# Performance work log

Measured on AMD Instinct MI355X. Metric: run time of the kernel, lower is better.

## Reference

```python
import jax, jax.numpy as jnp
import numpy as np

D_MODEL = 2048
H = 16
D_K = D_MODEL // H


def setup_inputs() -> dict:
    key = jax.random.key(0)
    ks = jax.random.split(key, 9)
    b, n, d = 2, 2048, D_MODEL
    s = 1.0 / np.sqrt(d)
    return {
        "x": jax.random.normal(ks[0], (b, n, d), jnp.float32),
        "Wq": jax.random.normal(ks[1], (d, d), jnp.float32) * s,
        "bq": jax.random.normal(ks[2], (d,), jnp.float32) * 0.01,
        "Wk": jax.random.normal(ks[3], (d, d), jnp.float32) * s,
        "bk": jax.random.normal(ks[4], (d,), jnp.float32) * 0.01,
        "Wv": jax.random.normal(ks[5], (d, d), jnp.float32) * s,
        "bv": jax.random.normal(ks[6], (d,), jnp.float32) * 0.01,
        "Wo": jax.random.normal(ks[7], (d, d), jnp.float32) * s,
        "bo": jax.random.normal(ks[8], (d,), jnp.float32) * 0.01,
    }


def reference(x, Wq, bq, Wk, bk, Wv, bv, Wo, bo):
    b, n, d = x.shape
    h, dk = H, D_K

    def split_heads(t):
        return t.reshape(b, n, h, dk).transpose(0, 2, 1, 3)  # (b,h,n,dk)

    q = split_heads(x @ Wq + bq)
    k = split_heads(x @ Wk + bk)
    v = split_heads(x @ Wv + bv)

    scores = jnp.einsum("bhqd,bhkd->bhqk", q, k) / jnp.sqrt(jnp.float32(dk))
    causal = jnp.tril(jnp.ones((n, n), dtype=bool))  # (n,n)
    scores = jnp.where(causal[None, None], scores, -jnp.inf)
    attn = jax.nn.softmax(scores, axis=-1)  # dropout = identity (eval)

    out = jnp.einsum("bhqk,bhkd->bhqd", attn, v)
    out = out.transpose(0, 2, 1, 3).reshape(b, n, d)
    return out @ Wo + bo
```

## Files before the change

### kernel.cpp

```cpp
#include <hip/hip_runtime.h>

typedef unsigned short u16;
typedef unsigned int u32;
typedef __attribute__((ext_vector_type(8))) short short8;
typedef __attribute__((ext_vector_type(4))) float f32x4;
typedef __attribute__((ext_vector_type(16))) float f32x16;
typedef __attribute__((ext_vector_type(4))) u16 u16x4;
typedef __attribute__((ext_vector_type(4))) u32 u32x4;

#define QK_SCALE 0.12751736915185197f

__device__ __forceinline__ u16 f2bf(float f) {
  u32 u = __builtin_bit_cast(u32, f);
  u = u + 0x7FFFu + ((u >> 16) & 1u);
  return (u16)(u >> 16);
}

__device__ __forceinline__ void async_copy16(const void* g, void* l) {
  __builtin_amdgcn_global_load_lds(
      (const __attribute__((address_space(1))) u32*)g,
      (__attribute__((address_space(3))) u32*)l, 16, 0, 0);
}

#define VMCNT(n) asm volatile("s_waitcnt vmcnt(" #n ")" ::: "memory")

__global__ __launch_bounds__(256) void cast_x_kernel(const float* __restrict__ x,
                                                     u16* __restrict__ xb, int n) {
  int i = (blockIdx.x * 256 + threadIdx.x) * 8;
  if (i >= n) return;
  float4 a = *(const float4*)(x + i);
  float4 b = *(const float4*)(x + i + 4);
  short8 o;
  o[0] = (short)f2bf(a.x); o[1] = (short)f2bf(a.y);
  o[2] = (short)f2bf(a.z); o[3] = (short)f2bf(a.w);
  o[4] = (short)f2bf(b.x); o[5] = (short)f2bf(b.y);
  o[6] = (short)f2bf(b.z); o[7] = (short)f2bf(b.w);
  *(short8*)(xb + i) = o;
}

__global__ __launch_bounds__(256) void transW_kernel(
    const float* __restrict__ W0, const float* __restrict__ W1,
    const float* __restrict__ W2, const float* __restrict__ W3,
    u16* __restrict__ O0, u16* __restrict__ O1, u16* __restrict__ O2, u16* __restrict__ O3) {
  const float* Ws[4] = {W0, W1, W2, W3};
  u16* Os[4] = {O0, O1, O2, O3};
  const float* W = Ws[blockIdx.z];
  u16* O = Os[blockIdx.z];

  __shared__ float T[64][65];
  int t = threadIdx.x;
  int k0 = blockIdx.y * 64, n0 = blockIdx.x * 64;
  int r = t >> 4, c = (t & 15) * 4;
#pragma unroll
  for (int i = 0; i < 4; ++i) {
    float4 v = *(const float4*)&W[(size_t)(k0 + r + i * 16) * 2048 + n0 + c];
    T[r + i * 16][c + 0] = v.x; T[r + i * 16][c + 1] = v.y;
    T[r + i * 16][c + 2] = v.z; T[r + i * 16][c + 3] = v.w;
  }
  __syncthreads();
#pragma unroll
  for (int i = 0; i < 4; ++i) {
    int nn = r + i * 16;
    u16x4 o;
    o[0] = f2bf(T[c + 0][nn]); o[1] = f2bf(T[c + 1][nn]);
    o[2] = f2bf(T[c + 2][nn]); o[3] = f2bf(T[c + 3][nn]);
    *(u16x4*)&O[(size_t)(n0 + nn) * 2048 + k0 + c] = o;
  }
}

__global__ __launch_bounds__(512, 1) void gemm256_kernel(
    const u16* __restrict__ A, const u16* __restrict__ W,
    const float* __restrict__ b0, const float* __restrict__ b1, const float* __restrict__ b2,
    u16* __restrict__ oq, u16* __restrict__ ok, u16* __restrict__ ovt) {
  __shared__ __align__(16) u16 SM[67584];

  int t = threadIdx.x;
  int lane = t & 63, w = t >> 6;
  int wm = w >> 2, wn = w & 3;
  int g = lane >> 4, lr = lane & 15;
  int m0 = blockIdx.y * 256, n0 = blockIdx.x * 256;

  const u16* AsrcB = A + (size_t)(m0 + (t >> 3)) * 2048 + ((t & 7) ^ ((t >> 3) & 7)) * 8;
  const u16* BsrcB = W + (size_t)(n0 + (t >> 3)) * 2048 + ((t & 7) ^ ((t >> 3) & 7)) * 8;
  int t8 = t * 8;

  int ko0 = (g ^ (lr & 7)) * 8;
  int ko1 = ((4 + g) ^ (lr & 7)) * 8;
  int aoff[8], boff[4];
#pragma unroll
  for (int mf = 0; mf < 8; ++mf) aoff[mf] = (wm * 128 + mf * 16 + lr) * 64;
#pragma unroll
  for (int nf = 0; nf < 4; ++nf) boff[nf] = (wn * 64 + nf * 16 + lr) * 64;

  f32x4 acc[8][4] = {};
  short8 af[2][2], bfr[4][2];

#define SA(b, j, tl) \
  async_copy16(AsrcB + (size_t)(j) * 131072 + (tl) * 64, (void*)(SM + (b) * 32768 + (j) * 4096 + t8))
#define SB(b, j, tl) \
  async_copy16(BsrcB + (size_t)(j) * 131072 + (tl) * 64, \
               (void*)(SM + (b) * 32768 + 16384 + (j) * 4096 + t8))

#define PHASE(hbuf, q, STAGE_OPS, VM_OP)                                        \
  {                                                                             \
    const u16* Ab = SM + (hbuf) * 32768;                                        \
    const u16* Bb = Ab + 16384;                                                 \
    af[0][0] = *(const short8*)&Ab[aoff[2 * (q)] + ko0];                        \
    af[0][1] = *(const short8*)&Ab[aoff[2 * (q)] + ko1];                        \
    af[1][0] = *(const short8*)&Ab[aoff[2 * (q) + 1] + ko0];                    \
    af[1][1] = *(const short8*)&Ab[aoff[2 * (q) + 1] + ko1];                    \
    if ((q) == 0) {                                                             \
      _Pragma("unroll") for (int nf = 0; nf < 4; ++nf) {                        \
        bfr[nf][0] = *(const short8*)&Bb[boff[nf] + ko0];                       \
        bfr[nf][1] = *(const short8*)&Bb[boff[nf] + ko1];                       \
      }                                                                         \
    }                                                                           \
    STAGE_OPS;                                                                  \
    __builtin_amdgcn_s_barrier();                                               \
    asm volatile("s_waitcnt lgkmcnt(0)" ::: "memory");                          \
    __builtin_amdgcn_sched_barrier(0);                                          \
    __builtin_amdgcn_s_setprio(1);                                              \
    _Pragma("unroll") for (int kk = 0; kk < 2; ++kk)                            \
        _Pragma("unroll") for (int m2 = 0; m2 < 2; ++m2)                        \
            _Pragma("unroll") for (int nf = 0; nf < 4; ++nf)                    \
                acc[2 * (q) + m2][nf] = __builtin_amdgcn_mfma_f32_16x16x32_bf16(\
                    af[m2][kk], bfr[nf][kk], acc[2 * (q) + m2][nf], 0, 0, 0);   \
    __builtin_amdgcn_s_setprio(0);                                              \
    VM_OP;                                                                      \
    __builtin_amdgcn_s_barrier();                                               \
  }

  SB(0, 0, 0); SB(0, 1, 0); SB(0, 2, 0); SB(0, 3, 0);
  SA(0, 0, 0); SA(0, 2, 0); SA(0, 1, 0); SA(0, 3, 0);
  SB(1, 0, 1); SB(1, 1, 1); SB(1, 2, 1); SB(1, 3, 1);
  SA(1, 0, 1); SA(1, 2, 1);
  VMCNT(6);
  __builtin_amdgcn_s_barrier();

  for (int i = 0; i < 16; ++i) {
    bool more = i < 15;
    int t1 = 2 * i + 1, t2 = 2 * i + 2, t3 = 2 * i + 3;
    PHASE(0, 0, { SA(1, 1, t1); SA(1, 3, t1); }, {});
    PHASE(0, 1, { if (more) { SB(0, 0, t2); SB(0, 1, t2); } }, {});
    PHASE(0, 2, { if (more) { SB(0, 2, t2); SB(0, 3, t2); } }, {});
    PHASE(0, 3, { if (more) { SA(0, 0, t2); SA(0, 2, t2); } },
          { if (more) { VMCNT(6); } else { VMCNT(0); } });
    PHASE(1, 0, { if (more) { SA(0, 1, t2); SA(0, 3, t2); } }, {});
    PHASE(1, 1, { if (more) { SB(1, 0, t3); SB(1, 1, t3); } }, {});
    PHASE(1, 2, { if (more) { SB(1, 2, t3); SB(1, 3, t3); } }, {});
    PHASE(1, 3, { if (more) { SA(1, 0, t3); SA(1, 2, t3); } },
          { if (more) { VMCNT(6); } else { VMCNT(0); } });
  }
#undef PHASE
#undef SA
#undef SB

  int zsel = n0 >> 11;
  const float* bias = (zsel == 0) ? b0 : (zsel == 1) ? b1 : b2;
  bool isV = (zsel == 2);

#pragma unroll
  for (int mf = 0; mf < 8; ++mf) {
#pragma unroll
    for (int nf = 0; nf < 4; ++nf) {
      int colc = wn * 64 + nf * 16 + lr;
      float bv = bias[(n0 + colc) & 2047];
#pragma unroll
      for (int i = 0; i < 4; ++i) {
        int token = wm * 128 + mf * 16 + 4 * g + i;
        u16 v = f2bf(acc[mf][nf][i] + bv);
        if (isV) SM[colc * 264 + token] = v;
        else SM[token * 264 + colc] = v;
      }
    }
  }
  __syncthreads();

  if (!isV) {
    u16* outb = (zsel == 0) ? oq : ok;
#pragma unroll
    for (int it = 0; it < 16; ++it) {
      int id = t + 512 * it;
      int token = id >> 5, c8 = (id & 31) * 8;
      short8 v = *(const short8*)&SM[token * 264 + c8];
      int rr = m0 + token;
      int colg = ((n0 + c8) & 2047);
      int b = rr >> 11, np = rr & 2047, h = colg >> 7, dk = colg & 127;
      *(short8*)&outb[((size_t)(b * 16 + h) * 2048 + np) * 128 + dk] = v;
    }
  } else {
#pragma unroll
    for (int it = 0; it < 16; ++it) {
      int id = t + 512 * it;
      int colc = id >> 5, t8k = (id & 31) * 8;
      short8 v = *(const short8*)&SM[colc * 264 + t8k];
      int rr = m0 + t8k;
      int vcol = (n0 - 4096) + colc;
      int b = rr >> 11, np = rr & 2047, h = vcol >> 7, dk = vcol & 127;
      *(short8*)&ovt[(((size_t)(b * 16 + h) * 128 + dk) * 2048) + np] = v;
    }
  }
}

__global__ __launch_bounds__(512, 2) void gemmO_kernel(
    const u16* __restrict__ A, const u16* __restrict__ W,
    const float* __restrict__ bias, float* __restrict__ of) {
  __shared__ __align__(16) u16 SM[73728];

  int t = threadIdx.x;
  int lane = t & 63, w = t >> 6;
  int wm = w >> 2, wn = w & 3;
  int g = lane >> 4, lr = lane & 15;
  int m0 = blockIdx.y * 128, n0 = blockIdx.x * 256;

  int sArow = ((t >> 8) << 6) + ((t >> 3) & 31);
  int c8A = (t & 7) ^ ((t >> 3) & 7);
  const u16* Asrc = A + (size_t)(m0 + sArow) * 2048 + c8A * 8;
  int rB = t >> 3;
  int c8B = (t & 7) ^ (rB & 7);
  const u16* Bsrc = W + (size_t)(n0 + rB) * 2048 + c8B * 8;

  int ko0 = (g ^ (lr & 7)) * 8;
  int ko1 = ((4 + g) ^ (lr & 7)) * 8;
  int offA[4], offB[4];
#pragma unroll
  for (int mf = 0; mf < 4; ++mf)
    offA[mf] = (mf >> 1) * 4096 + wm * 2048 + ((mf & 1) * 16 + lr) * 64;
#pragma unroll
  for (int nf = 0; nf < 4; ++nf)
    offB[nf] = 8192 + (wn >> 1) * 8192 + ((wn & 1) * 64 + nf * 16 + lr) * 64;

  f32x4 acc[4][4] = {};

#define STG_A(sbuf, mh, kt) \
  async_copy16(Asrc + (mh) * 65536 + (kt), (void*)(SM + (sbuf) + (mh) * 4096 + t * 8))
#define STG_B(sbuf, half, kt)                                                 \
  do {                                                                        \
    async_copy16(Bsrc + (half) * 262144 + (kt),                               \
                 (void*)(SM + (sbuf) + 8192 + (half) * 8192 + t * 8));        \
    async_copy16(Bsrc + (half) * 262144 + 131072 + (kt),                      \
                 (void*)(SM + (sbuf) + 8192 + (half) * 8192 + 4096 + t * 8)); \
  } while (0)

  STG_A(0, 0, 0); STG_B(0, 0, 0);
  STG_A(0, 1, 0); STG_B(0, 1, 0);
  STG_A(24576, 0, 64); STG_B(24576, 0, 64);
  STG_A(24576, 1, 64); STG_B(24576, 1, 64);
  VMCNT(6);
  __builtin_amdgcn_s_barrier();

  u32 cb = 0, sb = 49152;
  for (int tt = 0; tt < 32; ++tt) {
    int kt2 = (tt + 2) << 6;
    bool stg = tt < 30;
    const u16* Bu = SM + cb;

    short8 af[2][2], bfr[4][2];
#pragma unroll
    for (int m2 = 0; m2 < 2; ++m2) {
      af[m2][0] = *(const short8*)&Bu[offA[m2] + ko0];
      af[m2][1] = *(const short8*)&Bu[offA[m2] + ko1];
    }
#pragma unroll
    for (int nf = 0; nf < 4; ++nf) {
      bfr[nf][0] = *(const short8*)&Bu[offB[nf] + ko0];
      bfr[nf][1] = *(const short8*)&Bu[offB[nf] + ko1];
    }
    if (stg) { STG_A(sb, 0, kt2); STG_B(sb, 0, kt2); }
    __builtin_amdgcn_s_barrier();
    asm volatile("s_waitcnt lgkmcnt(0)" ::: "memory");
    __builtin_amdgcn_sched_barrier(0);
    __builtin_amdgcn_s_setprio(1);
#pragma unroll
    for (int kk = 0; kk < 2; ++kk)
#pragma unroll
      for (int m2 = 0; m2 < 2; ++m2)
#pragma unroll
        for (int nf = 0; nf < 4; ++nf)
          acc[m2][nf] =
              __builtin_amdgcn_mfma_f32_16x16x32_bf16(af[m2][kk], bfr[nf][kk], acc[m2][nf], 0, 0, 0);
    __builtin_amdgcn_s_setprio(0);
    __builtin_amdgcn_s_barrier();

#pragma unroll
    for (int m2 = 0; m2 < 2; ++m2) {
      af[m2][0] = *(const short8*)&Bu[offA[2 + m2] + ko0];
      af[m2][1] = *(const short8*)&Bu[offA[2 + m2] + ko1];
    }
    if (stg) { STG_A(sb, 1, kt2); STG_B(sb, 1, kt2); }
    __builtin_amdgcn_s_barrier();
    asm volatile("s_waitcnt lgkmcnt(0)" ::: "memory");
    __builtin_amdgcn_sched_barrier(0);
    __builtin_amdgcn_s_setprio(1);
#pragma unroll
    for (int kk = 0; kk < 2; ++kk)
#pragma unroll
      for (int m2 = 0; m2 < 2; ++m2)
#pragma unroll
        for (int nf = 0; nf < 4; ++nf)
          acc[2 + m2][nf] = __builtin_amdgcn_mfma_f32_16x16x32_bf16(af[m2][kk], bfr[nf][kk],
                                                                    acc[2 + m2][nf], 0, 0, 0);
    __builtin_amdgcn_s_setprio(0);
    if (tt < 30) { VMCNT(6); } else { VMCNT(0); }
    __builtin_amdgcn_s_barrier();

    cb += 24576; if (cb == 73728) cb = 0;
    sb += 24576; if (sb == 73728) sb = 0;
  }
#undef STG_A
#undef STG_B

#pragma unroll
  for (int mf = 0; mf < 4; ++mf) {
#pragma unroll
    for (int nf = 0; nf < 4; ++nf) {
      int col = n0 + wn * 64 + nf * 16 + lr;
      float bv = bias[col];
#pragma unroll
      for (int i = 0; i < 4; ++i) {
        int rr = m0 + wm * 64 + mf * 16 + 4 * g + i;
        of[(size_t)rr * 2048 + col] = acc[mf][nf][i] + bv;
      }
    }
  }
}

__global__ __launch_bounds__(256, 2) void attn_kernel(
    const u16* __restrict__ Q, const u16* __restrict__ K, const u16* __restrict__ Vt,
    u16* __restrict__ ctx) {
  int bh = blockIdx.y;
  int q0 = (int)(gridDim.x - 1 - blockIdx.x) * 128;
  int t = threadIdx.x, lane = t & 63, w = t >> 6;
  int h = lane >> 5;
  int ql = lane & 31;
  int q0w = q0 + w * 32;
  int qg = q0w + ql;

  const u16* Qb = Q + (size_t)bh * 262144;
  const u16* Kb = K + (size_t)bh * 262144;
  const u16* Vb = Vt + (size_t)bh * 262144;

  __shared__ __align__(16) u16 SM[32768];

  short8 qf[8];
  {
    const u16* qrow = Qb + (size_t)qg * 128 + 8 * h;
#pragma unroll
    for (int kk = 0; kk < 8; ++kk) qf[kk] = *(const short8*)(qrow + 16 * kk);
  }

  f32x16 acc[4] = {};
  float m = -1e30f, lsum = 0.f;

  int nt = (q0 + 128) >> 6;
  int wave_max = q0w + 31;

  auto STAGE = [&](int buf, int kv0) {
    u16* Ksb = SM + buf * 16384;
    u16* Vsb = Ksb + 8192;
#pragma unroll
    for (int it = 0; it < 4; ++it) {
      int p = t + 256 * it;
      int row = p >> 4;
      int c = (p & 15) ^ (row & 15);
      async_copy16(Kb + (size_t)(kv0 + row) * 128 + c * 8, (void*)(Ksb + p * 8));
      async_copy16(Vb + (size_t)(2 * row + (c >> 3)) * 2048 + kv0 + (c & 7) * 8,
                   (void*)(Vsb + p * 8));
    }
  };

  STAGE(0, 0);
  __syncthreads();

  for (int step = 0; step < nt; ++step) {
    int kv0 = step << 6;
    int cur = step & 1;
    if (step + 1 < nt) STAGE(cur ^ 1, (step + 1) << 6);

    if (kv0 <= wave_max) {
      const u16* Ksb = SM + cur * 16384;
      const u16* Vsb = Ksb + 8192;

      f32x16 s0 = {}, s1 = {};
      __builtin_amdgcn_s_setprio(1);
#pragma unroll
      for (int kk = 0; kk < 8; ++kk) {
        int c = (2 * kk + h) ^ (ql & 15);
        short8 kf0 = *(const short8*)&Ksb[ql * 128 + c * 8];
        s0 = __builtin_amdgcn_mfma_f32_32x32x16_bf16(kf0, qf[kk], s0, 0, 0, 0);
        short8 kf1 = *(const short8*)&Ksb[(32 + ql) * 128 + c * 8];
        s1 = __builtin_amdgcn_mfma_f32_32x32x16_bf16(kf1, qf[kk], s1, 0, 0, 0);
      }
      __builtin_amdgcn_s_setprio(0);

      if (kv0 + 63 > q0w) {
#pragma unroll
        for (int r = 0; r < 16; ++r) {
          int slot = (r & 3) + 8 * (r >> 2) + 4 * h;
          if (kv0 + slot > qg) s0[r] = -1e30f;
          if (kv0 + 32 + slot > qg) s1[r] = -1e30f;
        }
      }

      float tm = fmaxf(s0[0], s1[0]);
#pragma unroll
      for (int r = 1; r < 16; ++r) tm = fmaxf(tm, fmaxf(s0[r], s1[r]));
      tm = fmaxf(tm, __shfl_xor(tm, 32));
      tm *= QK_SCALE;

      if (__any(tm > m + 8.0f)) {
        float mn = fmaxf(m, tm);
        float rr = exp2f(m - mn);
        m = mn;
        lsum *= rr;
#pragma unroll
        for (int d = 0; d < 4; ++d)
#pragma unroll
          for (int i = 0; i < 16; ++i) acc[d][i] *= rr;
      }

      float rs = 0.f;
#pragma unroll
      for (int r = 0; r < 16; ++r) {
        s0[r] = exp2f(fmaf(s0[r], QK_SCALE, -m));
        s1[r] = exp2f(fmaf(s1[r], QK_SCALE, -m));
        rs += s0[r] + s1[r];
      }
      rs += __shfl_xor(rs, 32);
      lsum += rs;

      u32 up0[8], up1[8];
#pragma unroll
      for (int mi = 0; mi < 8; ++mi) {
        asm("v_cvt_pk_bf16_f32 %0, %1, %2" : "=v"(up0[mi]) : "v"(s0[2 * mi]), "v"(s0[2 * mi + 1]));
        asm("v_cvt_pk_bf16_f32 %0, %1, %2" : "=v"(up1[mi]) : "v"(s1[2 * mi]), "v"(s1[2 * mi + 1]));
      }

#pragma unroll
      for (int g16 = 0; g16 < 4; ++g16) {
        int Qd = g16 & 1;
        u32 c0 = (g16 < 2) ? up0[4 * Qd + 0] : up1[4 * Qd + 0];
        u32 c1 = (g16 < 2) ? up0[4 * Qd + 1] : up1[4 * Qd + 1];
        u32 c2 = (g16 < 2) ? up0[4 * Qd + 2] : up1[4 * Qd + 2];
        u32 c3 = (g16 < 2) ? up0[4 * Qd + 3] : up1[4 * Qd + 3];
        u32 d0 = __shfl_xor(c0, 32), d1 = __shfl_xor(c1, 32);
        u32 d2 = __shfl_xor(c2, 32), d3 = __shfl_xor(c3, 32);
        u32x4 paw;
        paw[0] = h ? d2 : c0;
        paw[1] = h ? d3 : c1;
        paw[2] = h ? c2 : d0;
        paw[3] = h ? c3 : d1;
        short8 pa = __builtin_bit_cast(short8, paw);
        __builtin_amdgcn_s_setprio(1);
#pragma unroll
        for (int d = 0; d < 4; ++d) {
          int dk = 32 * d + ql;
          int prow = dk >> 1;
          int lch = (dk & 1) * 8 + 2 * g16 + h;
          int slot = lch ^ (prow & 15);
          short8 vf = *(const short8*)&Vsb[prow * 128 + slot * 8];
          acc[d] = __builtin_amdgcn_mfma_f32_32x32x16_bf16(vf, pa, acc[d], 0, 0, 0);
        }
        __builtin_amdgcn_s_setprio(0);
      }
    }
    __syncthreads();
  }

  u16* Ot = SM + w * 4352;
  float inv = 1.f / lsum;
#pragma unroll
  for (int d = 0; d < 4; ++d)
#pragma unroll
    for (int r = 0; r < 16; ++r) {
      int dk = 32 * d + (r & 3) + 8 * (r >> 2) + 4 * h;
      Ot[ql * 136 + dk] = f2bf(acc[d][r] * inv);
    }
  __syncthreads();
  int b = bh >> 4, hh = bh & 15;
#pragma unroll
  for (int it = 0; it < 8; ++it) {
    int p = lane + 64 * it;
    int row = p >> 4, ch = p & 15;
    short8 v = *(const short8*)&Ot[row * 136 + ch * 8];
    *(short8*)(ctx + ((size_t)(b * 2048 + q0 + w * 32 + row)) * 2048 + hh * 128 + ch * 8) = v;
  }
}

extern "C" void kernel_launch(void* const* d_in, const int* in_sizes, int n_in,
                              void* d_out, int out_size, void* d_ws, size_t ws_size,
                              hipStream_t stream) {
  const float* x = (const float*)d_in[0];
  const float* Wq = (const float*)d_in[1];
  const float* bq = (const float*)d_in[2];
  const float* Wk = (const float*)d_in[3];
  const float* bk = (const float*)d_in[4];
  const float* Wv = (const float*)d_in[5];
  const float* bv = (const float*)d_in[6];
  const float* Wo = (const float*)d_in[7];
  const float* bo = (const float*)d_in[8];
  float* out = (float*)d_out;

  u16* xb = (u16*)d_ws;
  u16* WTq = xb + 8388608;
  u16* WTk = WTq + 4194304;
  u16* WTv = WTk + 4194304;
  u16* WTo = WTv + 4194304;
  u16* Qs = WTo + 4194304;
  u16* Ks = Qs + 8388608;
  u16* Vt = Ks + 8388608;
  u16* ctx = Vt + 8388608;

  cast_x_kernel<<<4096, 256, 0, stream>>>(x, xb, 8388608);
  transW_kernel<<<dim3(32, 32, 4), 256, 0, stream>>>(Wq, Wk, Wv, Wo, WTq, WTk, WTv, WTo);
  gemm256_kernel<<<dim3(24, 16), 512, 0, stream>>>(xb, WTq, bq, bk, bv, Qs, Ks, Vt);
  attn_kernel<<<dim3(16, 32), 256, 0, stream>>>(Qs, Ks, Vt, ctx);
  gemmO_kernel<<<dim3(8, 32), 512, 0, stream>>>(ctx, WTo, bo, out);
}
```

Baseline: 266.4 us.

## Shrink QKV GEMM tile to 256x192 to balance grid across CUs

The fused QKV projection GEMM now uses 256x192 tiles instead of 256x256, launching 512 blocks instead of 384 with a smaller LDS footprint and launch bounds that allow two blocks per CU. The aim is to fill the 256 CUs in whole waves and improve occupancy. Because tiles can now straddle the Q/K/V boundaries, the epilogue writes Q and K directly from registers with scalar stores and stages only the V columns through LDS for the transpose. The cost is lower arithmetic intensity per tile and uncoalesced 2-byte stores for Q and K.

After: 250.5 us. -6.0%, faster.

```diff
diff --git a/kernel.cpp b/kernel.cpp
--- a/kernel.cpp
+++ b/kernel.cpp
@@ -68,17 +68,17 @@
   }
 }
 
-__global__ __launch_bounds__(512, 1) void gemm256_kernel(
+__global__ __launch_bounds__(512, 2) void gemm192_kernel(
     const u16* __restrict__ A, const u16* __restrict__ W,
     const float* __restrict__ b0, const float* __restrict__ b1, const float* __restrict__ b2,
     u16* __restrict__ oq, u16* __restrict__ ok, u16* __restrict__ ovt) {
-  __shared__ __align__(16) u16 SM[67584];
+  __shared__ __align__(16) u16 SM[57344];
 
   int t = threadIdx.x;
   int lane = t & 63, w = t >> 6;
   int wm = w >> 2, wn = w & 3;
   int g = lane >> 4, lr = lane & 15;
-  int m0 = blockIdx.y * 256, n0 = blockIdx.x * 256;
+  int m0 = blockIdx.y * 256, n0 = blockIdx.x * 192;
 
   const u16* AsrcB = A + (size_t)(m0 + (t >> 3)) * 2048 + ((t & 7) ^ ((t >> 3) & 7)) * 8;
   const u16* BsrcB = W + (size_t)(n0 + (t >> 3)) * 2048 + ((t & 7) ^ ((t >> 3) & 7)) * 8;
@@ -86,33 +86,32 @@
 
   int ko0 = (g ^ (lr & 7)) * 8;
   int ko1 = ((4 + g) ^ (lr & 7)) * 8;
-  int aoff[8], boff[4];
+  int aoff[8], boff[3];
 #pragma unroll
   for (int mf = 0; mf < 8; ++mf) aoff[mf] = (wm * 128 + mf * 16 + lr) * 64;
 #pragma unroll
-  for (int nf = 0; nf < 4; ++nf) boff[nf] = (wn * 64 + nf * 16 + lr) * 64;
-
-  f32x4 acc[8][4] = {};
-  short8 af[2][2], bfr[4][2];
-
-#define SA(b, j, tl) \
-  async_copy16(AsrcB + (size_t)(j) * 131072 + (tl) * 64, (void*)(SM + (b) * 32768 + (j) * 4096 + t8))
-#define SB(b, j, tl) \
+  for (int nf = 0; nf < 3; ++nf) boff[nf] = 16384 + (wn * 48 + nf * 16 + lr) * 64;
+
+  f32x4 acc[8][3] = {};
+  short8 af[2][2], bfr[3][2];
+
+#define SA(bb, j, tl) \
+  async_copy16(AsrcB + (size_t)(j) * 131072 + (tl) * 64, (void*)(SM + (bb) * 28672 + (j) * 4096 + t8))
+#define SB(bb, j, tl) \
   async_copy16(BsrcB + (size_t)(j) * 131072 + (tl) * 64, \
-               (void*)(SM + (b) * 32768 + 16384 + (j) * 4096 + t8))
+               (void*)(SM + (bb) * 28672 + 16384 + (j) * 4096 + t8))
 
 #define PHASE(hbuf, q, STAGE_OPS, VM_OP)                                        \
   {                                                                             \
-    const u16* Ab = SM + (hbuf) * 32768;                                        \
-    const u16* Bb = Ab + 16384;                                                 \
+    const u16* Ab = SM + (hbuf) * 28672;                                        \
     af[0][0] = *(const short8*)&Ab[aoff[2 * (q)] + ko0];                        \
     af[0][1] = *(const short8*)&Ab[aoff[2 * (q)] + ko1];                        \
     af[1][0] = *(const short8*)&Ab[aoff[2 * (q) + 1] + ko0];                    \
     af[1][1] = *(const short8*)&Ab[aoff[2 * (q) + 1] + ko1];                    \
     if ((q) == 0) {                                                             \
-      _Pragma("unroll") for (int nf = 0; nf < 4; ++nf) {                        \
-        bfr[nf][0] = *(const short8*)&Bb[boff[nf] + ko0];                       \
-        bfr[nf][1] = *(const short8*)&Bb[boff[nf] + ko1];                       \
+      _Pragma("unroll") for (int nf = 0; nf < 3; ++nf) {                        \
+        bfr[nf][0] = *(const short8*)&Ab[boff[nf] + ko0];                       \
+        bfr[nf][1] = *(const short8*)&Ab[boff[nf] + ko1];                       \
       }                                                                         \
     }                                                                           \
     STAGE_OPS;                                                                  \
@@ -122,7 +121,7 @@
     __builtin_amdgcn_s_setprio(1);                                              \
     _Pragma("unroll") for (int kk = 0; kk < 2; ++kk)                            \
         _Pragma("unroll") for (int m2 = 0; m2 < 2; ++m2)                        \
-            _Pragma("unroll") for (int nf = 0; nf < 4; ++nf)                    \
+            _Pragma("unroll") for (int nf = 0; nf < 3; ++nf)                    \
                 acc[2 * (q) + m2][nf] = __builtin_amdgcn_mfma_f32_16x16x32_bf16(\
                     af[m2][kk], bfr[nf][kk], acc[2 * (q) + m2][nf], 0, 0, 0);   \
     __builtin_amdgcn_s_setprio(0);                                              \
@@ -130,11 +129,11 @@
     __builtin_amdgcn_s_barrier();                                               \
   }
 
-  SB(0, 0, 0); SB(0, 1, 0); SB(0, 2, 0); SB(0, 3, 0);
-  SA(0, 0, 0); SA(0, 2, 0); SA(0, 1, 0); SA(0, 3, 0);
-  SB(1, 0, 1); SB(1, 1, 1); SB(1, 2, 1); SB(1, 3, 1);
+  SB(0, 0, 0); SB(0, 1, 0); SB(0, 2, 0);
+  SA(0, 0, 0); SA(0, 1, 0); SA(0, 2, 0); SA(0, 3, 0);
+  SB(1, 0, 1); SB(1, 1, 1); SB(1, 2, 1);
   SA(1, 0, 1); SA(1, 2, 1);
-  VMCNT(6);
+  VMCNT(5);
   __builtin_amdgcn_s_barrier();
 
   for (int i = 0; i < 16; ++i) {
@@ -142,62 +141,63 @@
     int t1 = 2 * i + 1, t2 = 2 * i + 2, t3 = 2 * i + 3;
     PHASE(0, 0, { SA(1, 1, t1); SA(1, 3, t1); }, {});
     PHASE(0, 1, { if (more) { SB(0, 0, t2); SB(0, 1, t2); } }, {});
-    PHASE(0, 2, { if (more) { SB(0, 2, t2); SB(0, 3, t2); } }, {});
-    PHASE(0, 3, { if (more) { SA(0, 0, t2); SA(0, 2, t2); } },
-          { if (more) { VMCNT(6); } else { VMCNT(0); } });
+    PHASE(0, 2, { if (more) { SB(0, 2, t2); SA(0, 0, t2); } }, {});
+    PHASE(0, 3, { if (more) { SA(0, 2, t2); } },
+          { if (more) { VMCNT(5); } else { VMCNT(0); } });
     PHASE(1, 0, { if (more) { SA(0, 1, t2); SA(0, 3, t2); } }, {});
     PHASE(1, 1, { if (more) { SB(1, 0, t3); SB(1, 1, t3); } }, {});
-    PHASE(1, 2, { if (more) { SB(1, 2, t3); SB(1, 3, t3); } }, {});
-    PHASE(1, 3, { if (more) { SA(1, 0, t3); SA(1, 2, t3); } },
-          { if (more) { VMCNT(6); } else { VMCNT(0); } });
+    PHASE(1, 2, { if (more) { SB(1, 2, t3); SA(1, 0, t3); } }, {});
+    PHASE(1, 3, { if (more) { SA(1, 2, t3); } },
+          { if (more) { VMCNT(5); } else { VMCNT(0); } });
   }
 #undef PHASE
 #undef SA
 #undef SB
 
-  int zsel = n0 >> 11;
-  const float* bias = (zsel == 0) ? b0 : (zsel == 1) ? b1 : b2;
-  bool isV = (zsel == 2);
-
+  bool hasV = (n0 + 191) >= 4096;
 #pragma unroll
   for (int mf = 0; mf < 8; ++mf) {
 #pragma unroll
-    for (int nf = 0; nf < 4; ++nf) {
-      int colc = wn * 64 + nf * 16 + lr;
-      float bv = bias[(n0 + colc) & 2047];
-#pragma unroll
-      for (int i = 0; i < 4; ++i) {
-        int token = wm * 128 + mf * 16 + 4 * g + i;
-        u16 v = f2bf(acc[mf][nf][i] + bv);
-        if (isV) SM[colc * 264 + token] = v;
-        else SM[token * 264 + colc] = v;
-      }
-    }
-  }
-  __syncthreads();
-
-  if (!isV) {
-    u16* outb = (zsel == 0) ? oq : ok;
-#pragma unroll
-    for (int it = 0; it < 16; ++it) {
+    for (int nf = 0; nf < 3; ++nf) {
+      int colc = wn * 48 + nf * 16 + lr;
+      int col = n0 + colc;
+      int z = col >> 11;
+      int cc = col & 2047;
+      if (z < 2) {
+        float bv = (z == 0 ? b0 : b1)[cc];
+        u16* outb = (z == 0) ? oq : ok;
+#pragma unroll
+        for (int i = 0; i < 4; ++i) {
+          int rr = m0 + wm * 128 + mf * 16 + 4 * g + i;
+          int b = rr >> 11, np = rr & 2047, h = cc >> 7, dk = cc & 127;
+          outb[((size_t)(b * 16 + h) * 2048 + np) * 128 + dk] = f2bf(acc[mf][nf][i] + bv);
+        }
+      } else {
+        float bv = b2[cc];
+#pragma unroll
+        for (int i = 0; i < 4; ++i) {
+          int token = wm * 128 + mf * 16 + 4 * g + i;
+          SM[colc * 264 + token] = f2bf(acc[mf][nf][i] + bv);
+        }
+      }
+    }
+  }
+  if (hasV) {
+    __syncthreads();
+    int b = m0 >> 11;
+    int npb = m0 & 2047;
+#pragma unroll
+    for (int it = 0; it < 12; ++it) {
       int id = t + 512 * it;
-      int token = id >> 5, c8 = (id & 31) * 8;
-      short8 v = *(const short8*)&SM[token * 264 + c8];
-      int rr = m0 + token;
-      int colg = ((n0 + c8) & 2047);
-      int b = rr >> 11, np = rr & 2047, h = colg >> 7, dk = colg & 127;
-      *(short8*)&outb[((size_t)(b * 16 + h) * 2048 + np) * 128 + dk] = v;
-    }
-  } else {
-#pragma unroll
-    for (int it = 0; it < 16; ++it) {
-      int id = t + 512 * it;
-      int colc = id >> 5, t8k = (id & 31) * 8;
-      short8 v = *(const short8*)&SM[colc * 264 + t8k];
-      int rr = m0 + t8k;
-      int vcol = (n0 - 4096) + colc;
-      int b = rr >> 11, np = rr & 2047, h = vcol >> 7, dk = vcol & 127;
-      *(short8*)&ovt[(((size_t)(b * 16 + h) * 128 + dk) * 2048) + np] = v;
+      int colc = id >> 5;
+      int c8 = (id & 31) * 8;
+      int col = n0 + colc;
+      if (col >= 4096) {
+        short8 v = *(const short8*)&SM[colc * 264 + c8];
+        int vcol = col - 4096;
+        int h = vcol >> 7, dk = vcol & 127;
+        *(short8*)&ovt[(((size_t)(b * 16 + h) * 128 + dk) * 2048) + npb + c8] = v;
+      }
     }
   }
 }
@@ -513,7 +513,7 @@
 
   cast_x_kernel<<<4096, 256, 0, stream>>>(x, xb, 8388608);
   transW_kernel<<<dim3(32, 32, 4), 256, 0, stream>>>(Wq, Wk, Wv, Wo, WTq, WTk, WTv, WTo);
-  gemm256_kernel<<<dim3(24, 16), 512, 0, stream>>>(xb, WTq, bq, bk, bv, Qs, Ks, Vt);
+  gemm192_kernel<<<dim3(32, 16), 512, 0, stream>>>(xb, WTq, bq, bk, bv, Qs, Ks, Vt);
   attn_kernel<<<dim3(16, 32), 256, 0, stream>>>(Qs, Ks, Vt, ctx);
   gemmO_kernel<<<dim3(8, 32), 512, 0, stream>>>(ctx, WTo, bo, out);
 }
```
